# Optimization experiments

Measured on AMD Instinct MI355X. Metric: run time of the kernel, lower is better.

The kernel has to match this reference:

```python
import jax, jax.numpy as jnp
import numpy as np

B, S, SE, D, H, F1, I, E, ND = 8, 512, 512, 1024, 16, 4096, 1024, 8, 4

def _ln(x, g, b, eps=1e-5):
    mu = x.mean(-1, keepdims=True)
    var = ((x - mu) ** 2).mean(-1, keepdims=True)
    return (x - mu) * jax.lax.rsqrt(var + eps) * g + b

def _mha(q_in, kv_in, qw, qb, kw, kb, vw, vb, ow, ob):
    b, sq, d = q_in.shape
    sk = kv_in.shape[1]
    dh = d // H
    scale = dh ** -0.5
    q = ((q_in @ qw.T + qb) * scale).reshape(b, sq, H, dh)
    k = (kv_in @ kw.T + kb).reshape(b, sk, H, dh)
    v = (kv_in @ vw.T + vb).reshape(b, sk, H, dh)
    attn = jax.nn.softmax(jnp.einsum('bqhd,bkhd->bhqk', q, k), axis=-1)
    o = jnp.einsum('bhqk,bkhd->bqhd', attn, v).reshape(b, sq, d)
    return o @ ow.T + ob

def setup_inputs():
    key = jax.random.key(0)
    ks = jax.random.split(key, 40)
    p = lambda i, sh: jax.random.normal(ks[i], sh, jnp.float32) * 0.02
    return {
        'hidden_states': jax.random.normal(ks[0], (B, S, D), jnp.float32),
        'encoder_hidden_states': jax.random.normal(ks[1], (B, SE, D), jnp.float32),
        'idxes': jax.random.randint(ks[2], (B,), 0, ND),
        'sa_qw': p(3, (D, D)), 'sa_qb': p(4, (D,)), 'sa_kw': p(5, (D, D)), 'sa_kb': p(6, (D,)),
        'sa_vw': p(7, (D, D)), 'sa_vb': p(8, (D,)), 'sa_ow': p(9, (D, D)), 'sa_ob': p(10, (D,)),
        'ca_qw': p(11, (D, D)), 'ca_qb': p(12, (D,)), 'ca_kw': p(13, (D, D)), 'ca_kb': p(14, (D,)),
        'ca_vw': p(15, (D, D)), 'ca_vb': p(16, (D,)), 'ca_ow': p(17, (D, D)), 'ca_ob': p(18, (D,)),
        'sa_ln_g': jnp.ones((D,), jnp.float32), 'sa_ln_b': jnp.zeros((D,), jnp.float32),
        'ca_ln_g': jnp.ones((D,), jnp.float32), 'ca_ln_b': jnp.zeros((D,), jnp.float32),
        'fin_ln_g': jnp.ones((D,), jnp.float32), 'fin_ln_b': jnp.zeros((D,), jnp.float32),
        'fc1_w': p(19, (F1, D)), 'fc1_b': p(20, (F1,)),
        'fc2_w': p(21, (D, F1)), 'fc2_b': p(22, (D,)),
        'exp1_w': p(23, (E, I, D)), 'exp1_b': p(24, (E, I)),
        'exp2_w': p(25, (E, D, I)),
        'gate_w': p(26, (ND, E, D)), 'gate_b': p(27, (ND, E)),
    }

def reference(hidden_states, encoder_hidden_states, idxes, sa_qw, sa_qb, sa_kw, sa_kb, sa_vw, sa_vb, sa_ow, sa_ob, ca_qw, ca_qb, ca_kw, ca_kb, ca_vw, ca_vb, ca_ow, ca_ob, sa_ln_g, sa_ln_b, ca_ln_g, ca_ln_b, fin_ln_g, fin_ln_b, fc1_w, fc1_b, fc2_w, fc2_b, exp1_w, exp1_b, exp2_w, gate_w, gate_b):
    # self-attention block
    res = hidden_states
    h = _mha(hidden_states, hidden_states, sa_qw, sa_qb, sa_kw, sa_kb, sa_vw, sa_vb, sa_ow, sa_ob)
    h = _ln(res + h, sa_ln_g, sa_ln_b)
    # cross-attention block
    res = h
    h = _mha(h, encoder_hidden_states, ca_qw, ca_qb, ca_kw, ca_kb, ca_vw, ca_vb, ca_ow, ca_ob)
    h = _ln(res + h, ca_ln_g, ca_ln_b)
    # dataset-gated MoE FFN (dropout=0 eval, margin_loss=False, keep_resident=True)
    bsz, seq, d = h.shape
    x = h.reshape(-1, d)                              # [T, D]
    tok_ds = jnp.repeat(idxes, seq)                   # [T] dataset id per token
    logits = jnp.einsum('ted,td->te', gate_w[tok_ds], x) + gate_b[tok_ds]
    probs = jax.nn.softmax(logits, axis=-1)
    gate = jnp.argmax(probs, axis=-1)                 # top-1 expert per token
    gate_value = jnp.max(probs, axis=-1)
    oh = jax.nn.one_hot(gate, E, dtype=x.dtype)       # [T, E] dispatch mask
    # effective expert fc1 = concat(fc1, expert_fc1): shared half + per-token expert half
    h1 = jax.nn.gelu(x @ fc1_w.T + fc1_b, approximate=False)                                  # [T, F1]
    h2 = jax.nn.gelu(jnp.einsum('td,te,eid->ti', x, oh, exp1_w) + exp1_b[gate], approximate=False)  # [T, I]
    # effective expert fc2 = concat(fc2, expert_fc2, dim=1), shared fc2 bias
    out = h1 @ fc2_w.T + jnp.einsum('ti,te,edi->td', h2, oh, exp2_w) + fc2_b                  # [T, D]
    out = out * gate_value[:, None]                   # keep_resident: scale before residual
    out = _ln(x + out, fin_ln_g, fin_ln_b)
    return out.reshape(bsz, seq, d)
```

## Files before the change

### kernel.cpp

```cpp
#include <hip/hip_runtime.h>
#include <math.h>

constexpr int cS = 512, cD = 1024, cH = 16, cDH = 64;
constexpr int cF1 = 4096, cI = 1024, cE = 8;
constexpr int cT = 4096;
constexpr long long TD = (long long)cT * cD;
constexpr long long WW = 1048576;

typedef __attribute__((ext_vector_type(8))) short bfrag;
typedef _Float16 f16x8 __attribute__((ext_vector_type(8)));
typedef __attribute__((ext_vector_type(4))) float f32x4;

__device__ __forceinline__ float gelu_exact(float x) {
  return 0.5f * x * (1.0f + erff(x * 0.70710678118654752440f));
}
__device__ __forceinline__ unsigned short f2b_rne(float x) {
  union { float f; unsigned u; } v; v.f = x;
  unsigned r = v.u + 0x7fffu + ((v.u >> 16) & 1u);
  return (unsigned short)(r >> 16);
}
__device__ __forceinline__ void split2(float v, unsigned short& h, unsigned short& m) {
  _Float16 hh = (_Float16)v;
  float r = v - (float)hh;
  _Float16 mm = (_Float16)r;
  union { _Float16 f; unsigned short u; } a, b;
  a.f = hh; b.f = mm;
  h = a.u; m = b.u;
}
__device__ __forceinline__ void async16(const void* g, void* l) {
  __builtin_amdgcn_global_load_lds(
      (const __attribute__((address_space(1))) unsigned int*)g,
      (__attribute__((address_space(3))) unsigned int*)l, 16, 0, 0);
}
__device__ __forceinline__ float wsum(float v) {
#pragma unroll
  for (int off = 32; off; off >>= 1) v += __shfl_xor(v, off, 64);
  return v;
}
__device__ __forceinline__ float wmax(float v) {
#pragma unroll
  for (int off = 32; off; off >>= 1) v = fmaxf(v, __shfl_xor(v, off, 64));
  return v;
}

template<int BM, int BN, int NW, int WR, int OUT_MODE>
__global__ __launch_bounds__(NW * 64) void mgemm2(
    const unsigned short* __restrict__ Ap, long long aPS, long long sA, int lda,
    const unsigned short* __restrict__ Bp, long long bPS, long long sB, int ldb,
    const float* __restrict__ bias,
    void* __restrict__ Cp, long long sC, int ldc,
    int K, float alpha, int zbase)
{
  constexpr int WC = NW / WR;
  constexpr int WM = BM / WR, WN = BN / WC, AI = WM / 16, BJ = WN / 16;
  constexpr int CA = 2 * (BM / 16);
  constexpr int CB = 2 * (BN / 16);
  constexpr int CTOT = CA + CB;
  static_assert(CTOT % NW == 0, "chunk count");
  constexpr int NCH = CTOT / NW;
  constexpr int LT = (BM + BN) * 64;

  __shared__ unsigned short lds[2][LT];

  const int tid = threadIdx.x;
  const int w = tid >> 6, lane = tid & 63;
  const int z = blockIdx.z;
  const int m0 = blockIdx.x * BM, n0 = blockIdx.y * BN;
  const int wm = (w / WC) * WM, wn = (w % WC) * WN;
  const int lr = lane >> 2, lc8 = (lane & 3) * 8;

  const unsigned short* gsrc[NCH];
  int loff[NCH];
#pragma unroll
  for (int ci = 0; ci < NCH; ++ci) {
    const int c = w + ci * NW;
    if (c < CA) {
      const int p = c / (BM / 16), cc = c % (BM / 16);
      const int row = cc * 16 + lr;
      gsrc[ci] = Ap + p * aPS + (long long)z * sA + (long long)(m0 + row) * lda + lc8;
      loff[ci] = p * (BM * 32) + cc * (16 * 32);
    } else {
      const int cb = c - CA;
      const int p = cb / (BN / 16), cc = cb % (BN / 16);
      const int row = cc * 16 + lr;
      gsrc[ci] = Bp + p * bPS + (long long)z * sB + (long long)(n0 + row) * ldb + lc8;
      loff[ci] = 2 * (BM * 32) + p * (BN * 32) + cc * (16 * 32);
    }
  }

  f32x4 acc[AI][BJ];
#pragma unroll
  for (int i = 0; i < AI; ++i)
#pragma unroll
    for (int j = 0; j < BJ; ++j) acc[i][j] = (f32x4){0.f, 0.f, 0.f, 0.f};

#pragma unroll
  for (int ci = 0; ci < NCH; ++ci) async16(gsrc[ci], &lds[0][loff[ci]]);
  __syncthreads();

  int cur = 0;
  for (int k0 = 32; k0 <= K; k0 += 32) {
    if (k0 < K) {
#pragma unroll
      for (int ci = 0; ci < NCH; ++ci) async16(gsrc[ci] + k0, &lds[cur ^ 1][loff[ci]]);
    }
    const unsigned short* LA0 = &lds[cur][0];
    const unsigned short* LA1 = &lds[cur][BM * 32];
    const unsigned short* LB0 = &lds[cur][2 * (BM * 32)];
    const unsigned short* LB1 = &lds[cur][2 * (BM * 32) + BN * 32];

    f16x8 bf0[BJ], bf1[BJ], af[AI];
#pragma unroll
    for (int j = 0; j < BJ; ++j) {
      bf0[j] = *(const f16x8*)&LB0[(wn + j * 16 + (lane & 15)) * 32 + (lane >> 4) * 8];
      bf1[j] = *(const f16x8*)&LB1[(wn + j * 16 + (lane & 15)) * 32 + (lane >> 4) * 8];
    }
#pragma unroll
    for (int i = 0; i < AI; ++i)
      af[i] = *(const f16x8*)&LA0[(wm + i * 16 + (lane & 15)) * 32 + (lane >> 4) * 8];
#pragma unroll
    for (int i = 0; i < AI; ++i)
#pragma unroll
      for (int j = 0; j < BJ; ++j)
        acc[i][j] = __builtin_amdgcn_mfma_f32_16x16x32_f16(af[i], bf0[j], acc[i][j], 0, 0, 0);
#pragma unroll
    for (int i = 0; i < AI; ++i)
#pragma unroll
      for (int j = 0; j < BJ; ++j)
        acc[i][j] = __builtin_amdgcn_mfma_f32_16x16x32_f16(af[i], bf1[j], acc[i][j], 0, 0, 0);
#pragma unroll
    for (int i = 0; i < AI; ++i)
      af[i] = *(const f16x8*)&LA1[(wm + i * 16 + (lane & 15)) * 32 + (lane >> 4) * 8];
#pragma unroll
    for (int i = 0; i < AI; ++i)
#pragma unroll
      for (int j = 0; j < BJ; ++j)
        acc[i][j] = __builtin_amdgcn_mfma_f32_16x16x32_f16(af[i], bf0[j], acc[i][j], 0, 0, 0);
    __syncthreads();
    cur ^= 1;
  }

  const int zz = zbase + z;
#pragma unroll
  for (int i = 0; i < AI; ++i) {
#pragma unroll
    for (int r = 0; r < 4; ++r) {
      const int gm = m0 + wm + i * 16 + (lane >> 4) * 4 + r;
#pragma unroll
      for (int j = 0; j < BJ; ++j) {
        const int gn = n0 + wn + j * 16 + (lane & 15);
        float v = acc[i][j][r];
        if constexpr (OUT_MODE == 4) {
          v += bias[zz * cD + gn];
          unsigned short* C = (unsigned short*)Cp + (long long)zz * 2 * TD;
          const int b = gm >> 9, s = gm & 511, h = gn >> 6, dd = gn & 63;
          const long long idx = (((long long)(b * cH + h) * cS + s) << 6) + dd;
          unsigned short h_, m_;
          split2(v, h_, m_);
          C[idx] = h_; C[TD + idx] = m_;
        } else if constexpr (OUT_MODE == 5) {
          const int b = zz >> 4, h = zz & 15;
          const long long idx = ((long long)(b * cS + gm) << 10) + h * 64 + gn;
          unsigned short h_, m_;
          split2(v, h_, m_);
          ((unsigned short*)Cp)[idx] = h_;
          ((unsigned short*)Cp)[sC + idx] = m_;
        } else {
          if (bias) v += bias[gn];
          v *= alpha;
          const long long idx = (long long)z * sC + (long long)gm * ldc + gn;
          ((float*)Cp)[idx] = v;
        }
      }
    }
  }
}

__global__ __launch_bounds__(256) void transposeV(
    const unsigned short* __restrict__ src, unsigned short* __restrict__ dst)
{
  __shared__ unsigned short t[128 * 64];
  const int st = blockIdx.x;
  const int bh = blockIdx.y;
  const long long pl = (long long)blockIdx.z * TD;
  const unsigned short* Sp = src + pl + ((long long)bh * cS + st * 128) * cDH;
  const int tid = threadIdx.x;
  const int r0 = tid >> 3, c0 = (tid & 7) * 8;
#pragma unroll
  for (int i = 0; i < 4; ++i) {
    const int r = r0 + i * 32;
    uint4 v = *(const uint4*)(Sp + (long long)r * cDH + c0);
    *(uint4*)&t[r * 64 + (c0 ^ ((r & 7) << 3))] = v;
  }
  __syncthreads();
  const int dd = tid >> 2;
  unsigned short* Dp = dst + pl + (long long)(bh * cDH + dd) * cS + st * 128;
#pragma unroll
  for (int i = 0; i < 4; ++i) {
    const int s0 = ((tid & 3) + i * 4) * 8;
    alignas(16) unsigned short v[8];
#pragma unroll
    for (int j = 0; j < 8; ++j)
      v[j] = t[(s0 + j) * 64 + (dd ^ (j << 3))];
    *(uint4*)(Dp + s0) = *(const uint4*)v;
  }
}

template<int GATHER>
__global__ __launch_bounds__(256) void mgemm1(
    const unsigned short* __restrict__ A, int lda,
    const unsigned short* __restrict__ Bw, long long sB, int ldb,
    const float* __restrict__ bias, int sBias,
    void* __restrict__ Cp, int ldc,
    int K, int act, int obf, int accum,
    const int* __restrict__ token_list, const int* __restrict__ offsets)
{
  int m0, n0, beg = 0, cnt = 0x7fffffff;
  long long boff = 0;
  if constexpr (GATHER) {
    const int e = blockIdx.y;
    beg = offsets[e]; cnt = offsets[e + 1] - beg;
    m0 = blockIdx.z * 128;
    if (m0 >= cnt) return;
    n0 = blockIdx.x * 128;
    boff = (long long)e * sB;
    if (bias) bias += (long long)e * sBias;
  } else {
    m0 = blockIdx.x * 128; n0 = blockIdx.y * 128;
  }
  __shared__ unsigned short lds[2][256 * 32];
  const int tid = threadIdx.x, w = tid >> 6, lane = tid & 63;
  const int wm = (w >> 1) * 64, wn = (w & 1) * 64;
  const int lr = lane >> 2, lc8 = (lane & 3) * 8;

  const unsigned short* gsrc[4];
  int loff[4];
#pragma unroll
  for (int ci = 0; ci < 4; ++ci) {
    const int c = w + ci * 4;
    if (c < 8) {
      const int row = c * 16 + lr;
      long long grow;
      if constexpr (GATHER) {
        int mr = m0 + row; if (mr >= cnt) mr = cnt - 1;
        grow = token_list[beg + mr];
      } else grow = m0 + row;
      gsrc[ci] = A + grow * (long long)lda + lc8;
      loff[ci] = c * (16 * 32);
    } else {
      const int cc = c - 8;
      const int row = cc * 16 + lr;
      gsrc[ci] = Bw + boff + (long long)(n0 + row) * ldb + lc8;
      loff[ci] = 128 * 32 + cc * (16 * 32);
    }
  }
  f32x4 acc[4][4];
#pragma unroll
  for (int i = 0; i < 4; ++i)
#pragma unroll
    for (int j = 0; j < 4; ++j) acc[i][j] = (f32x4){0.f, 0.f, 0.f, 0.f};

#pragma unroll
  for (int ci = 0; ci < 4; ++ci) async16(gsrc[ci], &lds[0][loff[ci]]);
  __syncthreads();

  int cur = 0;
  for (int k0 = 32; k0 <= K; k0 += 32) {
    if (k0 < K) {
#pragma unroll
      for (int ci = 0; ci < 4; ++ci) async16(gsrc[ci] + k0, &lds[cur ^ 1][loff[ci]]);
    }
    const unsigned short* lA = &lds[cur][0];
    const unsigned short* lB = &lds[cur][128 * 32];
    bfrag af[4], bf[4];
#pragma unroll
    for (int i = 0; i < 4; ++i)
      af[i] = *(const bfrag*)&lA[(wm + i * 16 + (lane & 15)) * 32 + (lane >> 4) * 8];
#pragma unroll
    for (int j = 0; j < 4; ++j)
      bf[j] = *(const bfrag*)&lB[(wn + j * 16 + (lane & 15)) * 32 + (lane >> 4) * 8];
#pragma unroll
    for (int i = 0; i < 4; ++i)
#pragma unroll
      for (int j = 0; j < 4; ++j)
        acc[i][j] = __builtin_amdgcn_mfma_f32_16x16x32_bf16(af[i], bf[j], acc[i][j], 0, 0, 0);
    __syncthreads();
    cur ^= 1;
  }

#pragma unroll
  for (int i = 0; i < 4; ++i) {
#pragma unroll
    for (int r = 0; r < 4; ++r) {
      const int ml = wm + i * 16 + (lane >> 4) * 4 + r;
      long long orow = 0; bool ok = true;
      if constexpr (GATHER) {
        if (m0 + ml < cnt) orow = token_list[beg + m0 + ml]; else ok = false;
      } else orow = m0 + ml;
      if (ok) {
#pragma unroll
        for (int j = 0; j < 4; ++j) {
          const int gn = n0 + wn + j * 16 + (lane & 15);
          float v = acc[i][j][r];
          if (bias) v += bias[gn];
          if (act) v = gelu_exact(v);
          const long long idx = orow * (long long)ldc + gn;
          if (obf) ((unsigned short*)Cp)[idx] = f2b_rne(v);
          else if (accum) ((float*)Cp)[idx] += v;
          else ((float*)Cp)[idx] = v;
        }
      }
    }
  }
}

__global__ __launch_bounds__(256) void softmax2(
    const float* __restrict__ Sc, unsigned short* __restrict__ P, long long pPS)
{
  const int w = threadIdx.x >> 6, lane = threadIdx.x & 63;
  const long long row = (long long)blockIdx.x * 4 + w;
  const float* pr = Sc + row * cS + lane * 8;
  float4 a = *(const float4*)pr;
  float4 b = *(const float4*)(pr + 4);
  float e[8] = {a.x, a.y, a.z, a.w, b.x, b.y, b.z, b.w};
  float m = e[0];
#pragma unroll
  for (int q = 1; q < 8; ++q) m = fmaxf(m, e[q]);
  m = wmax(m);
  float s = 0.f;
#pragma unroll
  for (int q = 0; q < 8; ++q) { e[q] = expf(e[q] - m); s += e[q]; }
  s = wsum(s);
  const float inv = 1.0f / s;
  unsigned h[4], mm[4];
#pragma unroll
  for (int q = 0; q < 4; ++q) {
    unsigned short h0, m0s, h1, m1s;
    split2(e[2 * q] * inv, h0, m0s);
    split2(e[2 * q + 1] * inv, h1, m1s);
    h[q] = (unsigned)h0 | ((unsigned)h1 << 16);
    mm[q] = (unsigned)m0s | ((unsigned)m1s << 16);
  }
  const long long o = row * cS + lane * 8;
  *(uint4*)&P[o] = *(const uint4*)h;
  *(uint4*)&P[pPS + o] = *(const uint4*)mm;
}

__global__ __launch_bounds__(256) void addln_kernel(
    const float* __restrict__ ra, const float* __restrict__ rb,
    const float* __restrict__ rowscale,
    const float* __restrict__ g, const float* __restrict__ be,
    float* __restrict__ out, unsigned short* __restrict__ out16,
    unsigned short* __restrict__ out2p,
    int gate_on, const int* __restrict__ idxes,
    const float* __restrict__ gw, const float* __restrict__ gb,
    int* __restrict__ gate_idx, float* __restrict__ gate_val, int* __restrict__ counts)
{
  const int w = threadIdx.x >> 6, lane = threadIdx.x & 63;
  const int row = blockIdx.x * 4 + w;
  const long long base = (long long)row * cD + lane * 16;
  const float sc = rowscale ? rowscale[row] : 1.0f;
  float v[16];
#pragma unroll
  for (int q = 0; q < 4; ++q) {
    float4 a = *(const float4*)(ra + base + q * 4);
    float4 b = *(const float4*)(rb + base + q * 4);
    v[q * 4 + 0] = a.x + b.x * sc; v[q * 4 + 1] = a.y + b.y * sc;
    v[q * 4 + 2] = a.z + b.z * sc; v[q * 4 + 3] = a.w + b.w * sc;
  }
  float s = 0.f;
#pragma unroll
  for (int q = 0; q < 16; ++q) s += v[q];
  const float mu = wsum(s) * (1.0f / cD);
  float vp = 0.f;
#pragma unroll
  for (int q = 0; q < 16; ++q) { float c = v[q] - mu; vp += c * c; }
  const float rstd = 1.0f / sqrtf(wsum(vp) * (1.0f / cD) + 1e-5f);
  float x[16];
#pragma unroll
  for (int q = 0; q < 4; ++q) {
    float4 gv = *(const float4*)(g + lane * 16 + q * 4);
    float4 bv = *(const float4*)(be + lane * 16 + q * 4);
    x[q * 4 + 0] = (v[q * 4 + 0] - mu) * rstd * gv.x + bv.x;
    x[q * 4 + 1] = (v[q * 4 + 1] - mu) * rstd * gv.y + bv.y;
    x[q * 4 + 2] = (v[q * 4 + 2] - mu) * rstd * gv.z + bv.z;
    x[q * 4 + 3] = (v[q * 4 + 3] - mu) * rstd * gv.w + bv.w;
  }
  if (out) {
#pragma unroll
    for (int q = 0; q < 4; ++q) {
      float4 o; o.x = x[q * 4]; o.y = x[q * 4 + 1]; o.z = x[q * 4 + 2]; o.w = x[q * 4 + 3];
      *(float4*)(out + base + q * 4) = o;
    }
  }
  if (out16) {
    unsigned u[8];
#pragma unroll
    for (int q = 0; q < 8; ++q)
      u[q] = (unsigned)f2b_rne(x[2 * q]) | ((unsigned)f2b_rne(x[2 * q + 1]) << 16);
    *(uint4*)&out16[base] = *(const uint4*)&u[0];
    *(uint4*)&out16[base + 8] = *(const uint4*)&u[4];
  }
  if (out2p) {
    unsigned uh[8], um[8];
#pragma unroll
    for (int q = 0; q < 8; ++q) {
      unsigned short h0, m0s, h1, m1s;
      split2(x[2 * q], h0, m0s);
      split2(x[2 * q + 1], h1, m1s);
      uh[q] = (unsigned)h0 | ((unsigned)h1 << 16);
      um[q] = (unsigned)m0s | ((unsigned)m1s << 16);
    }
    *(uint4*)&out2p[base] = *(const uint4*)&uh[0];
    *(uint4*)&out2p[base + 8] = *(const uint4*)&uh[4];
    *(uint4*)&out2p[TD + base] = *(const uint4*)&um[0];
    *(uint4*)&out2p[TD + base + 8] = *(const uint4*)&um[4];
  }
  if (gate_on) {
    const int ds = idxes[row >> 9];
    const float* gwr = gw + (long long)ds * (cE * cD) + lane * 16;
    float glog[8];
#pragma unroll
    for (int e = 0; e < 8; ++e) {
      float pe = 0.f;
#pragma unroll
      for (int q = 0; q < 4; ++q) {
        float4 wv = *(const float4*)(gwr + e * cD + q * 4);
        pe += x[q * 4] * wv.x + x[q * 4 + 1] * wv.y + x[q * 4 + 2] * wv.z + x[q * 4 + 3] * wv.w;
      }
      glog[e] = wsum(pe);
    }
    if (lane == 0) {
      float m = glog[0] + gb[ds * cE];
      int arg = 0;
      float gl[8];
      gl[0] = m;
#pragma unroll
      for (int e = 1; e < 8; ++e) {
        gl[e] = glog[e] + gb[ds * cE + e];
        if (gl[e] > m) { m = gl[e]; arg = e; }
      }
      float ssum = 0.f;
#pragma unroll
      for (int e = 0; e < 8; ++e) ssum += expf(gl[e] - m);
      gate_idx[row] = arg;
      gate_val[row] = 1.0f / ssum;
      atomicAdd(&counts[arg], 1);
    }
  }
}

__global__ __launch_bounds__(256) void conv2x4(
    const float* s0, const float* s1, const float* s2, const float* s3,
    unsigned short* dst, int n, float sc0)
{
  const int wsel = blockIdx.y;
  const float* s = (wsel == 0) ? s0 : (wsel == 1) ? s1 : (wsel == 2) ? s2 : s3;
  const float sc = (wsel == 0) ? sc0 : 1.0f;
  unsigned short* d = dst + (long long)wsel * 2 * n;
  const long long i = ((long long)blockIdx.x * 256 + threadIdx.x) * 4;
  if (i >= n) return;
  float4 v = *(const float4*)(s + i);
  float vv[4] = {v.x * sc, v.y * sc, v.z * sc, v.w * sc};
  unsigned short h[4], m[4];
#pragma unroll
  for (int q = 0; q < 4; ++q) split2(vv[q], h[q], m[q]);
  uint2 u;
  u.x = (unsigned)h[0] | ((unsigned)h[1] << 16); u.y = (unsigned)h[2] | ((unsigned)h[3] << 16);
  *(uint2*)&d[i] = u;
  u.x = (unsigned)m[0] | ((unsigned)m[1] << 16); u.y = (unsigned)m[2] | ((unsigned)m[3] << 16);
  *(uint2*)&d[n + i] = u;
}

__global__ __launch_bounds__(256) void conv2p(const float* __restrict__ s,
                                              unsigned short* __restrict__ d, long long n)
{
  const long long i = ((long long)blockIdx.x * 256 + threadIdx.x) * 4;
  if (i >= n) return;
  float4 v = *(const float4*)(s + i);
  unsigned short h[4], m[4];
  split2(v.x, h[0], m[0]); split2(v.y, h[1], m[1]);
  split2(v.z, h[2], m[2]); split2(v.w, h[3], m[3]);
  uint2 u;
  u.x = (unsigned)h[0] | ((unsigned)h[1] << 16); u.y = (unsigned)h[2] | ((unsigned)h[3] << 16);
  *(uint2*)&d[i] = u;
  u.x = (unsigned)m[0] | ((unsigned)m[1] << 16); u.y = (unsigned)m[2] | ((unsigned)m[3] << 16);
  *(uint2*)&d[n + i] = u;
}

__global__ __launch_bounds__(256) void conv1(const float* __restrict__ s,
                                             unsigned short* __restrict__ d, long long n)
{
  const long long i = ((long long)blockIdx.x * 256 + threadIdx.x) * 4;
  if (i >= n) return;
  float4 v = *(const float4*)(s + i);
  uint2 u;
  u.x = (unsigned)f2b_rne(v.x) | ((unsigned)f2b_rne(v.y) << 16);
  u.y = (unsigned)f2b_rne(v.z) | ((unsigned)f2b_rne(v.w) << 16);
  *(uint2*)&d[i] = u;
}

__global__ void prep_bias(const float* a0, const float* a1, const float* a2,
                          const float* b0, const float* b1, const float* b2,
                          float* dst)
{
  const int i = blockIdx.x * 256 + threadIdx.x;
  const int seg = i >> 10, off = i & 1023;
  const float* srcs[6] = {a0, a1, a2, b0, b1, b2};
  const float sc = (seg == 0 || seg == 3) ? 0.125f : 1.0f;
  dst[i] = srcs[seg][off] * sc;
}

__global__ void scan_kernel(const int* __restrict__ counts, int* __restrict__ offsets,
                            int* __restrict__ cursor)
{
  if (threadIdx.x == 0 && blockIdx.x == 0) {
    int a = 0;
    for (int e = 0; e < cE; ++e) { offsets[e] = a; cursor[e] = a; a += counts[e]; }
    offsets[cE] = a;
  }
}

__global__ __launch_bounds__(256) void scatter_kernel(
    const int* __restrict__ gate_idx, int* __restrict__ cursor, int* __restrict__ token_list)
{
  int t = blockIdx.x * 256 + threadIdx.x;
  if (t < cT) {
    int e = gate_idx[t];
    int slot = atomicAdd(&cursor[e], 1);
    token_list[slot] = t;
  }
}

extern "C" void kernel_launch(void* const* d_in, const int* in_sizes, int n_in,
                              void* d_out, int out_size, void* d_ws, size_t ws_size,
                              hipStream_t stream)
{
  (void)in_sizes; (void)n_in; (void)out_size;
  const float* hidden  = (const float*)d_in[0];
  const float* encoder = (const float*)d_in[1];
  const int*   idxes   = (const int*)d_in[2];
  const float* sa_qw = (const float*)d_in[3];
  const float* sa_qb = (const float*)d_in[4];
  const float* sa_kw = (const float*)d_in[5];
  const float* sa_kb = (const float*)d_in[6];
  const float* sa_vw = (const float*)d_in[7];
  const float* sa_vb = (const float*)d_in[8];
  const float* sa_ow = (const float*)d_in[9];
  const float* sa_ob = (const float*)d_in[10];
  const float* ca_qw = (const float*)d_in[11];
  const float* ca_qb = (const float*)d_in[12];
  const float* ca_kw = (const float*)d_in[13];
  const float* ca_kb = (const float*)d_in[14];
  const float* ca_vw = (const float*)d_in[15];
  const float* ca_vb = (const float*)d_in[16];
  const float* ca_ow = (const float*)d_in[17];
  const float* ca_ob = (const float*)d_in[18];
  const float* sa_ln_g = (const float*)d_in[19];
  const float* sa_ln_b = (const float*)d_in[20];
  const float* ca_ln_g = (const float*)d_in[21];
  const float* ca_ln_b = (const float*)d_in[22];
  const float* fin_ln_g = (const float*)d_in[23];
  const float* fin_ln_b = (const float*)d_in[24];
  const float* fc1_w = (const float*)d_in[25];
  const float* fc1_b = (const float*)d_in[26];
  const float* fc2_w = (const float*)d_in[27];
  const float* fc2_b = (const float*)d_in[28];
  const float* exp1_w = (const float*)d_in[29];
  const float* exp1_b = (const float*)d_in[30];
  const float* exp2_w = (const float*)d_in[31];
  const float* gate_w = (const float*)d_in[32];
  const float* gate_b = (const float*)d_in[33];
  float* out = (float*)d_out;

  size_t off = 0;
  auto alloc = [&](size_t bytes) {
    void* p = (char*)d_ws + off;
    off += (bytes + 255) & ~(size_t)255;
    return p;
  };
  unsigned short* wbuf = (unsigned short*)alloc(4ll * 2 * WW * 2);
  unsigned short* QKVs = (unsigned short*)alloc(4ll * 2 * TD * 2);
  unsigned short* attnO16 = (unsigned short*)alloc(2ll * TD * 2);
  float* hsa   = (float*)alloc(TD * 4);
  float* biasb = (float*)alloc(6 * cD * 4);
  float* gate_val = (float*)alloc(cT * 4);
  int* gate_idx   = (int*)alloc(cT * 4);
  int* token_list = (int*)alloc(cT * 4);
  int* ctl        = (int*)alloc(64 * 4);
  int* counts  = ctl;
  int* offsets = ctl + 16;
  int* cursor  = ctl + 32;
  const size_t off_x = off;
  float* xbuf = (float*)alloc(TD * 4);
  unsigned short* x16 = (unsigned short*)alloc(TD * 2);

  long long region_bytes = (long long)ws_size - (long long)off_x;
  long long perz = (long long)cS * cS * 8;
  int ZB = (int)(region_bytes / perz);
  if (ZB < 1) ZB = 1;
  if (ZB > 128) ZB = 128;
  float* scoresF = (float*)((char*)d_ws + off_x);
  unsigned short* Pp = (unsigned short*)((char*)d_ws + off_x + (long long)ZB * cS * cS * 4);
  const long long pPS = (long long)ZB * cS * cS;

  unsigned short* A16 = QKVs + 6 * TD;
  unsigned short* hsa16 = attnO16;
  float* OdeltaF = (float*)QKVs;
  unsigned short* h2 = QKVs;
  float* moeF = (float*)(QKVs + 2 * WW * 4);
  unsigned short* h1 = QKVs + 16ll * WW;

  dim3 blk(256), blk512(512);
  hipMemsetAsync(counts, 0, cE * sizeof(int), stream);
  prep_bias<<<dim3(24), blk, 0, stream>>>(sa_qb, sa_kb, sa_vb, ca_qb, ca_kb, ca_vb, biasb);

  auto attention = [&]() {
    for (int zb = 0; zb < 128; zb += ZB) {
      int zc = 128 - zb; if (zc > ZB) zc = ZB;
      mgemm2<64, 256, 4, 1, 0><<<dim3(8, 2, zc), blk, 0, stream>>>(
          QKVs + (long long)zb * (cS * cDH), TD, (long long)cS * cDH, cDH,
          QKVs + 2 * TD + (long long)zb * (cS * cDH), TD, (long long)cS * cDH, cDH,
          nullptr, scoresF, (long long)cS * cS, cS, cDH, 1.0f, 0);
      softmax2<<<dim3(zc * cS / 4), blk, 0, stream>>>(scoresF, Pp, pPS);
      mgemm2<128, 64, 4, 2, 5><<<dim3(4, 1, zc), blk, 0, stream>>>(
          Pp, pPS, (long long)cS * cS, cS,
          QKVs + 6 * TD + (long long)zb * (cDH * cS), TD, (long long)cDH * cS, cS,
          nullptr, attnO16, TD, 0, cS, 1.0f, zb);
    }
  };

  conv2x4<<<dim3(1024, 4), blk, 0, stream>>>(sa_qw, sa_kw, sa_vw, sa_ow, wbuf, (int)WW, 0.125f);
  conv2p<<<dim3(4096), blk, 0, stream>>>(hidden, A16, TD);
  mgemm2<128, 256, 8, 2, 4><<<dim3(32, 4, 3), blk512, 0, stream>>>(
      A16, TD, 0, cD, wbuf, WW, 2 * WW, cD,
      biasb, QKVs, 0, 0, cD, 1.0f, 0);
  transposeV<<<dim3(4, 128, 2), blk, 0, stream>>>(QKVs + 4 * TD, QKVs + 6 * TD);
  attention();
  mgemm2<64, 256, 4, 1, 0><<<dim3(64, 4, 1), blk, 0, stream>>>(
      attnO16, TD, 0, cD, wbuf + 6ll * WW, WW, 0, cD,
      sa_ob, OdeltaF, 0, cD, cD, 1.0f, 0);
  addln_kernel<<<dim3(cT / 4), blk, 0, stream>>>(
      hidden, OdeltaF, nullptr, sa_ln_g, sa_ln_b, hsa, nullptr, hsa16,
      0, nullptr, nullptr, nullptr, nullptr, nullptr, nullptr);

  conv2x4<<<dim3(1024, 4), blk, 0, stream>>>(ca_qw, ca_kw, ca_vw, ca_ow, wbuf, (int)WW, 0.125f);
  mgemm2<64, 256, 4, 1, 4><<<dim3(64, 4, 1), blk, 0, stream>>>(
      hsa16, TD, 0, cD, wbuf, WW, 2 * WW, cD,
      biasb + 3 * cD, QKVs, 0, 0, cD, 1.0f, 0);
  conv2p<<<dim3(4096), blk, 0, stream>>>(encoder, A16, TD);
  mgemm2<128, 256, 8, 2, 4><<<dim3(32, 4, 2), blk512, 0, stream>>>(
      A16, TD, 0, cD, wbuf + 2ll * WW, WW, 2 * WW, cD,
      biasb + 3 * cD, QKVs, 0, 0, cD, 1.0f, 1);
  transposeV<<<dim3(4, 128, 2), blk, 0, stream>>>(QKVs + 4 * TD, QKVs + 6 * TD);
  attention();
  mgemm2<64, 256, 4, 1, 0><<<dim3(64, 4, 1), blk, 0, stream>>>(
      attnO16, TD, 0, cD, wbuf + 6ll * WW, WW, 0, cD,
      ca_ob, OdeltaF, 0, cD, cD, 1.0f, 0);
  addln_kernel<<<dim3(cT / 4), blk, 0, stream>>>(
      hsa, OdeltaF, nullptr, ca_ln_g, ca_ln_b, xbuf, x16, nullptr,
      1, idxes, gate_w, gate_b, gate_idx, gate_val, counts);

  scan_kernel<<<dim3(1), dim3(64), 0, stream>>>(counts, offsets, cursor);
  scatter_kernel<<<dim3(16), blk, 0, stream>>>(gate_idx, cursor, token_list);

  unsigned short* wfc1 = wbuf;
  unsigned short* wfc2 = wbuf + 4194304;
  conv1<<<dim3(4096), blk, 0, stream>>>(fc1_w, wfc1, 4194304);
  conv1<<<dim3(4096), blk, 0, stream>>>(fc2_w, wfc2, 4194304);
  mgemm1<0><<<dim3(32, 32), blk, 0, stream>>>(
      x16, cD, wfc1, 0, cD, fc1_b, 0,
      h1, cF1, cD, 1, 1, 0, nullptr, nullptr);
  mgemm1<0><<<dim3(32, 8), blk, 0, stream>>>(
      h1, cF1, wfc2, 0, cF1, fc2_b, 0,
      moeF, cD, cF1, 0, 0, 0, nullptr, nullptr);
  conv1<<<dim3(8192), blk, 0, stream>>>(exp1_w, wbuf, 8388608);
  mgemm1<1><<<dim3(8, 8, 32), blk, 0, stream>>>(
      x16, cD, wbuf, (long long)cI * cD, cD, exp1_b, cI,
      h2, cI, cD, 1, 1, 0, token_list, offsets);
  conv1<<<dim3(8192), blk, 0, stream>>>(exp2_w, wbuf, 8388608);
  mgemm1<1><<<dim3(8, 8, 32), blk, 0, stream>>>(
      h2, cI, wbuf, (long long)cD * cI, cI, nullptr, 0,
      moeF, cD, cI, 0, 0, 1, token_list, offsets);

  addln_kernel<<<dim3(cT / 4), blk, 0, stream>>>(
      xbuf, moeF, gate_val, fin_ln_g, fin_ln_b, out, nullptr, nullptr,
      0, nullptr, nullptr, nullptr, nullptr, nullptr, nullptr);
}
```

Before: 1.155 ms.

## Swizzle LDS tiles, set MFMA priority, and fuse QKV projections into one GEMM

Adds an XOR-swizzled LDS layout for both GEMM kernels so the fragment reads avoid bank conflicts. It wraps the MFMA blocks in s_setprio and adds explicit vmcnt waits before each barrier. It also changes the weight conversion so Q/K/V hi parts are contiguous, letting the QKV projections run as one wide-N GEMM with tsel-based output routing, and retunes the tile shapes of the projection and output GEMMs. The extra vmcnt waits could serialise the async prefetch with compute, and the new weight layout must agree with every consumer.

```diff
diff --git a/kernel.cpp b/kernel.cpp
--- a/kernel.cpp
+++ b/kernel.cpp
@@ -41,6 +41,10 @@
 #pragma unroll
   for (int off = 32; off; off >>= 1) v = fmaxf(v, __shfl_xor(v, off, 64));
   return v;
+}
+__device__ __forceinline__ int swzoff(int R, int c) {
+  const int r = R & 15;
+  return (R >> 4) * 512 + (r >> 1) * 64 + (((((r & 1) << 2) | c) ^ ((r >> 1) & 7)) << 3);
 }
 
 template<int BM, int BN, int NW, int WR, int OUT_MODE>
@@ -67,7 +71,9 @@
   const int z = blockIdx.z;
   const int m0 = blockIdx.x * BM, n0 = blockIdx.y * BN;
   const int wm = (w / WC) * WM, wn = (w % WC) * WN;
-  const int lr = lane >> 2, lc8 = (lane & 3) * 8;
+  const int sp = (lane & 7) ^ ((lane >> 3) & 7);
+  const int srow = ((lane >> 3) << 1) | (sp >> 2);
+  const int scol = (sp & 3) << 3;
 
   const unsigned short* gsrc[NCH];
   int loff[NCH];
@@ -76,15 +82,15 @@
     const int c = w + ci * NW;
     if (c < CA) {
       const int p = c / (BM / 16), cc = c % (BM / 16);
-      const int row = cc * 16 + lr;
-      gsrc[ci] = Ap + p * aPS + (long long)z * sA + (long long)(m0 + row) * lda + lc8;
-      loff[ci] = p * (BM * 32) + cc * (16 * 32);
+      const int row = cc * 16 + srow;
+      gsrc[ci] = Ap + p * aPS + (long long)z * sA + (long long)(m0 + row) * lda + scol;
+      loff[ci] = p * (BM * 32) + cc * 512;
     } else {
       const int cb = c - CA;
       const int p = cb / (BN / 16), cc = cb % (BN / 16);
-      const int row = cc * 16 + lr;
-      gsrc[ci] = Bp + p * bPS + (long long)z * sB + (long long)(n0 + row) * ldb + lc8;
-      loff[ci] = 2 * (BM * 32) + p * (BN * 32) + cc * (16 * 32);
+      const int row = cc * 16 + srow;
+      gsrc[ci] = Bp + p * bPS + (long long)z * sB + (long long)(n0 + row) * ldb + scol;
+      loff[ci] = 2 * (BM * 32) + p * (BN * 32) + cc * 512;
     }
   }
 
@@ -96,9 +102,11 @@
 
 #pragma unroll
   for (int ci = 0; ci < NCH; ++ci) async16(gsrc[ci], &lds[0][loff[ci]]);
+  asm volatile("s_waitcnt vmcnt(0)" ::: "memory");
   __syncthreads();
 
   int cur = 0;
+  const int lc = lane >> 4;
   for (int k0 = 32; k0 <= K; k0 += 32) {
     if (k0 < K) {
 #pragma unroll
@@ -112,12 +120,13 @@
     f16x8 bf0[BJ], bf1[BJ], af[AI];
 #pragma unroll
     for (int j = 0; j < BJ; ++j) {
-      bf0[j] = *(const f16x8*)&LB0[(wn + j * 16 + (lane & 15)) * 32 + (lane >> 4) * 8];
-      bf1[j] = *(const f16x8*)&LB1[(wn + j * 16 + (lane & 15)) * 32 + (lane >> 4) * 8];
+      bf0[j] = *(const f16x8*)&LB0[swzoff(wn + j * 16 + (lane & 15), lc)];
+      bf1[j] = *(const f16x8*)&LB1[swzoff(wn + j * 16 + (lane & 15), lc)];
     }
 #pragma unroll
     for (int i = 0; i < AI; ++i)
-      af[i] = *(const f16x8*)&LA0[(wm + i * 16 + (lane & 15)) * 32 + (lane >> 4) * 8];
+      af[i] = *(const f16x8*)&LA0[swzoff(wm + i * 16 + (lane & 15), lc)];
+    __builtin_amdgcn_s_setprio(1);
 #pragma unroll
     for (int i = 0; i < AI; ++i)
 #pragma unroll
@@ -128,19 +137,22 @@
 #pragma unroll
       for (int j = 0; j < BJ; ++j)
         acc[i][j] = __builtin_amdgcn_mfma_f32_16x16x32_f16(af[i], bf1[j], acc[i][j], 0, 0, 0);
+    __builtin_amdgcn_s_setprio(0);
 #pragma unroll
     for (int i = 0; i < AI; ++i)
-      af[i] = *(const f16x8*)&LA1[(wm + i * 16 + (lane & 15)) * 32 + (lane >> 4) * 8];
+      af[i] = *(const f16x8*)&LA1[swzoff(wm + i * 16 + (lane & 15), lc)];
+    __builtin_amdgcn_s_setprio(1);
 #pragma unroll
     for (int i = 0; i < AI; ++i)
 #pragma unroll
       for (int j = 0; j < BJ; ++j)
         acc[i][j] = __builtin_amdgcn_mfma_f32_16x16x32_f16(af[i], bf0[j], acc[i][j], 0, 0, 0);
+    __builtin_amdgcn_s_setprio(0);
+    asm volatile("s_waitcnt vmcnt(0)" ::: "memory");
     __syncthreads();
     cur ^= 1;
   }
 
-  const int zz = zbase + z;
 #pragma unroll
   for (int i = 0; i < AI; ++i) {
 #pragma unroll
@@ -151,14 +163,16 @@
         const int gn = n0 + wn + j * 16 + (lane & 15);
         float v = acc[i][j][r];
         if constexpr (OUT_MODE == 4) {
-          v += bias[zz * cD + gn];
-          unsigned short* C = (unsigned short*)Cp + (long long)zz * 2 * TD;
-          const int b = gm >> 9, s = gm & 511, h = gn >> 6, dd = gn & 63;
+          const int tsel = gn >> 10, gnn = gn & 1023;
+          v += bias[tsel * cD + gnn];
+          unsigned short* C = (unsigned short*)Cp + (long long)(zbase + tsel) * 2 * TD;
+          const int b = gm >> 9, s = gm & 511, h = gnn >> 6, dd = gnn & 63;
           const long long idx = (((long long)(b * cH + h) * cS + s) << 6) + dd;
           unsigned short h_, m_;
           split2(v, h_, m_);
           C[idx] = h_; C[TD + idx] = m_;
         } else if constexpr (OUT_MODE == 5) {
+          const int zz = zbase + z;
           const int b = zz >> 4, h = zz & 15;
           const long long idx = ((long long)(b * cS + gm) << 10) + h * 64 + gn;
           unsigned short h_, m_;
@@ -231,7 +245,9 @@
   __shared__ unsigned short lds[2][256 * 32];
   const int tid = threadIdx.x, w = tid >> 6, lane = tid & 63;
   const int wm = (w >> 1) * 64, wn = (w & 1) * 64;
-  const int lr = lane >> 2, lc8 = (lane & 3) * 8;
+  const int sp = (lane & 7) ^ ((lane >> 3) & 7);
+  const int srow = ((lane >> 3) << 1) | (sp >> 2);
+  const int scol = (sp & 3) << 3;
 
   const unsigned short* gsrc[4];
   int loff[4];
@@ -239,19 +255,19 @@
   for (int ci = 0; ci < 4; ++ci) {
     const int c = w + ci * 4;
     if (c < 8) {
-      const int row = c * 16 + lr;
+      const int row = c * 16 + srow;
       long long grow;
       if constexpr (GATHER) {
         int mr = m0 + row; if (mr >= cnt) mr = cnt - 1;
         grow = token_list[beg + mr];
       } else grow = m0 + row;
-      gsrc[ci] = A + grow * (long long)lda + lc8;
-      loff[ci] = c * (16 * 32);
+      gsrc[ci] = A + grow * (long long)lda + scol;
+      loff[ci] = c * 512;
     } else {
       const int cc = c - 8;
-      const int row = cc * 16 + lr;
-      gsrc[ci] = Bw + boff + (long long)(n0 + row) * ldb + lc8;
-      loff[ci] = 128 * 32 + cc * (16 * 32);
+      const int row = cc * 16 + srow;
+      gsrc[ci] = Bw + boff + (long long)(n0 + row) * ldb + scol;
+      loff[ci] = 128 * 32 + cc * 512;
     }
   }
   f32x4 acc[4][4];
@@ -262,9 +278,11 @@
 
 #pragma unroll
   for (int ci = 0; ci < 4; ++ci) async16(gsrc[ci], &lds[0][loff[ci]]);
+  asm volatile("s_waitcnt vmcnt(0)" ::: "memory");
   __syncthreads();
 
   int cur = 0;
+  const int lc = lane >> 4;
   for (int k0 = 32; k0 <= K; k0 += 32) {
     if (k0 < K) {
 #pragma unroll
@@ -275,15 +293,18 @@
     bfrag af[4], bf[4];
 #pragma unroll
     for (int i = 0; i < 4; ++i)
-      af[i] = *(const bfrag*)&lA[(wm + i * 16 + (lane & 15)) * 32 + (lane >> 4) * 8];
+      af[i] = *(const bfrag*)&lA[swzoff(wm + i * 16 + (lane & 15), lc)];
 #pragma unroll
     for (int j = 0; j < 4; ++j)
-      bf[j] = *(const bfrag*)&lB[(wn + j * 16 + (lane & 15)) * 32 + (lane >> 4) * 8];
+      bf[j] = *(const bfrag*)&lB[swzoff(wn + j * 16 + (lane & 15), lc)];
+    __builtin_amdgcn_s_setprio(1);
 #pragma unroll
     for (int i = 0; i < 4; ++i)
 #pragma unroll
       for (int j = 0; j < 4; ++j)
         acc[i][j] = __builtin_amdgcn_mfma_f32_16x16x32_bf16(af[i], bf[j], acc[i][j], 0, 0, 0);
+    __builtin_amdgcn_s_setprio(0);
+    asm volatile("s_waitcnt vmcnt(0)" ::: "memory");
     __syncthreads();
     cur ^= 1;
   }
@@ -457,7 +478,8 @@
   const int wsel = blockIdx.y;
   const float* s = (wsel == 0) ? s0 : (wsel == 1) ? s1 : (wsel == 2) ? s2 : s3;
   const float sc = (wsel == 0) ? sc0 : 1.0f;
-  unsigned short* d = dst + (long long)wsel * 2 * n;
+  unsigned short* dh = dst + (long long)(wsel < 3 ? wsel : 6) * n;
+  unsigned short* dm = dh + (long long)(wsel < 3 ? 3 : 1) * n;
   const long long i = ((long long)blockIdx.x * 256 + threadIdx.x) * 4;
   if (i >= n) return;
   float4 v = *(const float4*)(s + i);
@@ -467,9 +489,9 @@
   for (int q = 0; q < 4; ++q) split2(vv[q], h[q], m[q]);
   uint2 u;
   u.x = (unsigned)h[0] | ((unsigned)h[1] << 16); u.y = (unsigned)h[2] | ((unsigned)h[3] << 16);
-  *(uint2*)&d[i] = u;
+  *(uint2*)&dh[i] = u;
   u.x = (unsigned)m[0] | ((unsigned)m[1] << 16); u.y = (unsigned)m[2] | ((unsigned)m[3] << 16);
-  *(uint2*)&d[n + i] = u;
+  *(uint2*)&dm[i] = u;
 }
 
 __global__ __launch_bounds__(256) void conv2p(const float* __restrict__ s,
@@ -632,12 +654,12 @@
 
   conv2x4<<<dim3(1024, 4), blk, 0, stream>>>(sa_qw, sa_kw, sa_vw, sa_ow, wbuf, (int)WW, 0.125f);
   conv2p<<<dim3(4096), blk, 0, stream>>>(hidden, A16, TD);
-  mgemm2<128, 256, 8, 2, 4><<<dim3(32, 4, 3), blk512, 0, stream>>>(
-      A16, TD, 0, cD, wbuf, WW, 2 * WW, cD,
+  mgemm2<128, 192, 8, 2, 4><<<dim3(32, 16, 1), blk512, 0, stream>>>(
+      A16, TD, 0, cD, wbuf, 3 * WW, 0, cD,
       biasb, QKVs, 0, 0, cD, 1.0f, 0);
   transposeV<<<dim3(4, 128, 2), blk, 0, stream>>>(QKVs + 4 * TD, QKVs + 6 * TD);
   attention();
-  mgemm2<64, 256, 4, 1, 0><<<dim3(64, 4, 1), blk, 0, stream>>>(
+  mgemm2<128, 128, 4, 2, 0><<<dim3(32, 8, 1), blk, 0, stream>>>(
       attnO16, TD, 0, cD, wbuf + 6ll * WW, WW, 0, cD,
       sa_ob, OdeltaF, 0, cD, cD, 1.0f, 0);
   addln_kernel<<<dim3(cT / 4), blk, 0, stream>>>(
@@ -645,16 +667,16 @@
       0, nullptr, nullptr, nullptr, nullptr, nullptr, nullptr);
 
   conv2x4<<<dim3(1024, 4), blk, 0, stream>>>(ca_qw, ca_kw, ca_vw, ca_ow, wbuf, (int)WW, 0.125f);
-  mgemm2<64, 256, 4, 1, 4><<<dim3(64, 4, 1), blk, 0, stream>>>(
-      hsa16, TD, 0, cD, wbuf, WW, 2 * WW, cD,
+  mgemm2<128, 128, 4, 2, 4><<<dim3(32, 8, 1), blk, 0, stream>>>(
+      hsa16, TD, 0, cD, wbuf, 3 * WW, 0, cD,
       biasb + 3 * cD, QKVs, 0, 0, cD, 1.0f, 0);
   conv2p<<<dim3(4096), blk, 0, stream>>>(encoder, A16, TD);
-  mgemm2<128, 256, 8, 2, 4><<<dim3(32, 4, 2), blk512, 0, stream>>>(
-      A16, TD, 0, cD, wbuf + 2ll * WW, WW, 2 * WW, cD,
-      biasb + 3 * cD, QKVs, 0, 0, cD, 1.0f, 1);
+  mgemm2<128, 128, 4, 2, 4><<<dim3(32, 16, 1), blk, 0, stream>>>(
+      A16, TD, 0, cD, wbuf + WW, 3 * WW, 0, cD,
+      biasb + 4 * cD, QKVs, 0, 0, cD, 1.0f, 1);
   transposeV<<<dim3(4, 128, 2), blk, 0, stream>>>(QKVs + 4 * TD, QKVs + 6 * TD);
   attention();
-  mgemm2<64, 256, 4, 1, 0><<<dim3(64, 4, 1), blk, 0, stream>>>(
+  mgemm2<128, 128, 4, 2, 0><<<dim3(32, 8, 1), blk, 0, stream>>>(
       attnO16, TD, 0, cD, wbuf + 6ll * WW, WW, 0, cD,
       ca_ob, OdeltaF, 0, cD, cD, 1.0f, 0);
   addln_kernel<<<dim3(cT / 4), blk, 0, stream>>>(
```

Result: faster. 1.126 ms (-2.5%).
